# Kernel optimization log

Measured on AMD Instinct MI355X. Metric: run time of the kernel, lower is better.

## Reference

```python
import jax, jax.numpy as jnp
import numpy as np

B = 8192
TEXT_DIM = 2048
GRAPH_DIM = 1024
OUT_DIM = 1024
C = 2048  # common_dim = max(text_dim, graph_dim)
H = 16    # num_heads
LN_EPS = 1e-5


def _linear(x, W, b):
    # torch nn.Linear: y = x @ W.T + b, W: [out, in]
    return x @ W.T + b


def _mha(q, k, v, Wqkv, bqkv, Wo, bo):
    # Faithful to torch nn.MultiheadAttention (batch_first, eval mode).
    # Wqkv: [3C, C], bqkv: [3C], Wo: [C, C], bo: [C]
    Bq, S, _ = q.shape
    D = C // H
    Wq, Wk, Wv = Wqkv[:C], Wqkv[C:2 * C], Wqkv[2 * C:]
    bq, bk, bv = bqkv[:C], bqkv[C:2 * C], bqkv[2 * C:]
    qh = _linear(q, Wq, bq).reshape(Bq, S, H, D).transpose(0, 2, 1, 3)  # [B,H,S,D]
    kh = _linear(k, Wk, bk).reshape(Bq, S, H, D).transpose(0, 2, 1, 3)
    vh = _linear(v, Wv, bv).reshape(Bq, S, H, D).transpose(0, 2, 1, 3)
    scores = jnp.einsum('bhqd,bhkd->bhqk', qh, kh) / jnp.sqrt(jnp.asarray(D, qh.dtype))
    attn = jax.nn.softmax(scores, axis=-1)
    out = jnp.einsum('bhqk,bhkd->bhqd', attn, vh)
    out = out.transpose(0, 2, 1, 3).reshape(Bq, S, C)
    return _linear(out, Wo, bo)


def _layernorm(x, w, b):
    mu = jnp.mean(x, axis=-1, keepdims=True)
    var = jnp.mean(jnp.square(x - mu), axis=-1, keepdims=True)
    return (x - mu) * jax.lax.rsqrt(var + LN_EPS) * w + b


def setup_inputs() -> dict:
    key = jax.random.key(0)
    ks = jax.random.split(key, 16)
    s = 0.02
    return {
        'text_embeddings': jax.random.normal(ks[0], (B, TEXT_DIM), jnp.float32),
        'graph_embeddings': jax.random.normal(ks[1], (B, GRAPH_DIM), jnp.float32),
        'Wt': jax.random.normal(ks[2], (C, TEXT_DIM), jnp.float32) * s,
        'bt': jnp.zeros((C,), jnp.float32),
        'Wg': jax.random.normal(ks[3], (C, GRAPH_DIM), jnp.float32) * s,
        'bg': jnp.zeros((C,), jnp.float32),
        'Wqkv_s': jax.random.normal(ks[4], (3 * C, C), jnp.float32) * s,
        'bqkv_s': jnp.zeros((3 * C,), jnp.float32),
        'Wo_s': jax.random.normal(ks[5], (C, C), jnp.float32) * s,
        'bo_s': jnp.zeros((C,), jnp.float32),
        'Wqkv_c': jax.random.normal(ks[6], (3 * C, C), jnp.float32) * s,
        'bqkv_c': jnp.zeros((3 * C,), jnp.float32),
        'Wo_c': jax.random.normal(ks[7], (C, C), jnp.float32) * s,
        'bo_c': jnp.zeros((C,), jnp.float32),
        'ln_w': jnp.ones((C,), jnp.float32),
        'ln_b': jnp.zeros((C,), jnp.float32),
        'Wout': jax.random.normal(ks[8], (OUT_DIM, C), jnp.float32) * s,
        'bout': jnp.zeros((OUT_DIM,), jnp.float32),
    }


def reference(text_embeddings, graph_embeddings, Wt, bt, Wg, bg,
              Wqkv_s, bqkv_s, Wo_s, bo_s, Wqkv_c, bqkv_c, Wo_c, bo_c,
              ln_w, ln_b, Wout, bout):
    text_proj = _linear(text_embeddings, Wt, bt)    # [B, C]
    graph_proj = _linear(graph_embeddings, Wg, bg)  # [B, C]
    stacked = jnp.stack([text_proj, graph_proj], axis=1)  # [B, 2, C]
    attn_out = _mha(stacked, stacked, stacked, Wqkv_s, bqkv_s, Wo_s, bo_s)
    attn_out = _layernorm(attn_out, ln_w, ln_b)
    cross = _mha(attn_out, stacked, stacked, Wqkv_c, bqkv_c, Wo_c, bo_c)
    attn_out = attn_out + cross
    fused = jnp.mean(attn_out, axis=1)  # [B, C]
    return _linear(fused, Wout, bout)   # [B, OUT_DIM]
```

## Files before the change

kernel.cpp:

```cpp
#include <hip/hip_runtime.h>
#include <cstdio>

typedef unsigned short u16;
typedef float f32x4 __attribute__((ext_vector_type(4)));
typedef short s16x8 __attribute__((ext_vector_type(8)));

__device__ __forceinline__ u16 f2bf(float x) {
    unsigned u = __float_as_uint(x);
    u += 0x7fffu + ((u >> 16) & 1u);
    return (u16)(u >> 16);
}
__device__ __forceinline__ unsigned pack2(float a, float b) {
    return (unsigned)f2bf(a) | ((unsigned)f2bf(b) << 16);
}
__device__ __forceinline__ void unpack2(unsigned u, float& lo, float& hi) {
    lo = __uint_as_float(u << 16);
    hi = __uint_as_float(u & 0xffff0000u);
}

__device__ __forceinline__ void gl2lds16(const u16* g, u16* l) {
    __builtin_amdgcn_global_load_lds(
        (const __attribute__((address_space(1))) void*)g,
        (__attribute__((address_space(3))) void*)l, 16, 0, 0);
}

__device__ __forceinline__ uint4 ld8(const u16* p) { return *(const uint4*)p; }
__device__ __forceinline__ uint4 ld8(const float* p) {
    float4 a = ((const float4*)p)[0];
    float4 b = ((const float4*)p)[1];
    uint4 r;
    r.x = pack2(a.x, a.y);
    r.y = pack2(a.z, a.w);
    r.z = pack2(b.x, b.y);
    r.w = pack2(b.z, b.w);
    return r;
}

__global__ __launch_bounds__(256) void cast_f32_bf16(const float* __restrict__ x,
                                                     u16* __restrict__ y, int n4) {
    int i = blockIdx.x * 256 + threadIdx.x;
    if (i >= n4) return;
    float4 v = ((const float4*)x)[i];
    uint2 r;
    r.x = pack2(v.x, v.y);
    r.y = pack2(v.z, v.w);
    ((uint2*)y)[i] = r;
}

template <typename TA, typename TB, bool OUT_BF16>
__global__ __launch_bounds__(256) void gemm_bt(const TA* __restrict__ A,
                                               const TB* __restrict__ B,
                                               const float* __restrict__ bias,
                                               void* __restrict__ Cout,
                                               int K, int ldc) {
    __shared__ __align__(16) u16 As[128 * 32];
    __shared__ __align__(16) u16 Bs[128 * 32];

    const int tid = threadIdx.x;
    const int lane = tid & 63;
    const int wave = tid >> 6;
    const int wm = wave >> 1;
    const int wn = wave & 1;
    const size_t bm = (size_t)blockIdx.y * 128;
    const size_t bn = (size_t)blockIdx.x * 128;

    f32x4 acc[4][4];
#pragma unroll
    for (int i = 0; i < 4; ++i)
#pragma unroll
        for (int j = 0; j < 4; ++j) acc[i][j] = (f32x4)0.f;

    const int srow = tid >> 2;
    const int scol = (tid & 3) << 3;
    const TA* Ag = A + (bm + (size_t)srow) * K + scol;
    const TB* Bg = B + (bn + (size_t)srow) * K + scol;
    const size_t rstep = (size_t)64 * K;

    uint4 a0 = ld8(Ag);
    uint4 a1 = ld8(Ag + rstep);
    uint4 b0 = ld8(Bg);
    uint4 b1 = ld8(Bg + rstep);

    const int lrow = lane & 15;
    const int lk = (lane >> 4) << 3;

    const int niter = K >> 5;
    for (int t = 0; t < niter; ++t) {
        __syncthreads();
        *(uint4*)&As[srow * 32 + scol] = a0;
        *(uint4*)&As[(64 + srow) * 32 + scol] = a1;
        *(uint4*)&Bs[srow * 32 + scol] = b0;
        *(uint4*)&Bs[(64 + srow) * 32 + scol] = b1;
        __syncthreads();
        if (t + 1 < niter) {
            const int k0 = (t + 1) << 5;
            a0 = ld8(Ag + k0);
            a1 = ld8(Ag + rstep + k0);
            b0 = ld8(Bg + k0);
            b1 = ld8(Bg + rstep + k0);
        }
        s16x8 af[4], bfr[4];
#pragma unroll
        for (int i = 0; i < 4; ++i)
            af[i] = *(const s16x8*)&As[(wm * 64 + i * 16 + lrow) * 32 + lk];
#pragma unroll
        for (int j = 0; j < 4; ++j)
            bfr[j] = *(const s16x8*)&Bs[(wn * 64 + j * 16 + lrow) * 32 + lk];
#pragma unroll
        for (int i = 0; i < 4; ++i)
#pragma unroll
            for (int j = 0; j < 4; ++j)
                acc[i][j] = __builtin_amdgcn_mfma_f32_16x16x32_bf16(
                    af[i], bfr[j], acc[i][j], 0, 0, 0);
    }

    const size_t crow0 = bm + wm * 64 + ((lane >> 4) << 2);
    const int ccol0 = (int)bn + wn * 64 + (lane & 15);
#pragma unroll
    for (int i = 0; i < 4; ++i) {
#pragma unroll
        for (int j = 0; j < 4; ++j) {
            const int col = ccol0 + j * 16;
            const float bv = bias[col];
            const size_t base = (crow0 + (size_t)i * 16) * (size_t)ldc + col;
#pragma unroll
            for (int r = 0; r < 4; ++r) {
                const float v = acc[i][j][r] + bv;
                if (OUT_BF16)
                    ((u16*)Cout)[base + (size_t)r * ldc] = f2bf(v);
                else
                    ((float*)Cout)[base + (size_t)r * ldc] = v;
            }
        }
    }
}

template <bool OUT_BF16>
__global__ __launch_bounds__(256) void gemm_async(const u16* __restrict__ A, int lda,
                                                  const u16* __restrict__ B,
                                                  const float* __restrict__ bias,
                                                  void* __restrict__ Cout,
                                                  int K, int ldc) {
    __shared__ __align__(16) u16 As[128 * 32];
    __shared__ __align__(16) u16 Bs[128 * 32];

    const int tid = threadIdx.x;
    const int lane = tid & 63;
    const int wave = tid >> 6;
    const int wm = wave >> 1;
    const int wn = wave & 1;
    const size_t bm = (size_t)blockIdx.y * 128;
    const size_t bn = (size_t)blockIdx.x * 128;

    f32x4 acc[4][4];
#pragma unroll
    for (int i = 0; i < 4; ++i)
#pragma unroll
        for (int j = 0; j < 4; ++j) acc[i][j] = (f32x4)0.f;

    const int srow = tid >> 2;
    const int scol = (tid & 3) << 3;
    const u16* Ag = A + (bm + (size_t)srow) * (size_t)lda + scol;
    const u16* Bg = B + (bn + (size_t)srow) * (size_t)K + scol;
    const size_t rA = (size_t)64 * lda;
    const size_t rB = (size_t)64 * K;
    u16* lA0 = &As[tid * 8];
    u16* lA1 = &As[2048 + tid * 8];
    u16* lB0 = &Bs[tid * 8];
    u16* lB1 = &Bs[2048 + tid * 8];

    const int lrow = lane & 15;
    const int lk = (lane >> 4) << 3;

    const int niter = K >> 5;
    for (int t = 0; t < niter; ++t) {
        __syncthreads();
        gl2lds16(Ag, lA0);
        gl2lds16(Ag + rA, lA1);
        gl2lds16(Bg, lB0);
        gl2lds16(Bg + rB, lB1);
        Ag += 32;
        Bg += 32;
        __syncthreads();
        s16x8 af[4], bfr[4];
#pragma unroll
        for (int i = 0; i < 4; ++i)
            af[i] = *(const s16x8*)&As[(wm * 64 + i * 16 + lrow) * 32 + lk];
#pragma unroll
        for (int j = 0; j < 4; ++j)
            bfr[j] = *(const s16x8*)&Bs[(wn * 64 + j * 16 + lrow) * 32 + lk];
#pragma unroll
        for (int i = 0; i < 4; ++i)
#pragma unroll
            for (int j = 0; j < 4; ++j)
                acc[i][j] = __builtin_amdgcn_mfma_f32_16x16x32_bf16(
                    af[i], bfr[j], acc[i][j], 0, 0, 0);
    }

    const size_t crow0 = bm + wm * 64 + ((lane >> 4) << 2);
    const int ccol0 = (int)bn + wn * 64 + (lane & 15);
#pragma unroll
    for (int i = 0; i < 4; ++i) {
#pragma unroll
        for (int j = 0; j < 4; ++j) {
            const int col = ccol0 + j * 16;
            const float bv = bias[col];
            const size_t base = (crow0 + (size_t)i * 16) * (size_t)ldc + col;
#pragma unroll
            for (int r = 0; r < 4; ++r) {
                const float v = acc[i][j][r] + bv;
                if (OUT_BF16)
                    ((u16*)Cout)[base + (size_t)r * ldc] = f2bf(v);
                else
                    ((float*)Cout)[base + (size_t)r * ldc] = v;
            }
        }
    }
}

#define LDA_FRAG(mh)                                                          \
    do {                                                                      \
        _Pragma("unroll") for (int m = 0; m < 4; ++m) {                       \
            const u16* p = &As[cur][aBase + ((mh)*64 + m * 16) * 64];         \
            aF[m][0] = *(const s16x8*)(p + aK0);                              \
            aF[m][1] = *(const s16x8*)(p + aK1);                              \
        }                                                                     \
    } while (0)

#define LDB_FRAG(nh, bf)                                                      \
    do {                                                                      \
        _Pragma("unroll") for (int n = 0; n < 2; ++n) {                       \
            const u16* p = &Bs[cur][bBase + ((nh)*32 + n * 16) * 64];         \
            bf[n][0] = *(const s16x8*)(p + aK0);                              \
            bf[n][1] = *(const s16x8*)(p + aK1);                              \
        }                                                                     \
    } while (0)

#define STAGE_A(v, h)                                                         \
    do {                                                                      \
        u16* d = &As[(v)&1][(h)*8192 + tid * 8];                              \
        gl2lds16(aSrc[h][0] + (size_t)(v)*64, d);                             \
        gl2lds16(aSrc[h][1] + (size_t)(v)*64, d + 4096);                      \
    } while (0)

#define STAGE_B(v, h)                                                         \
    do {                                                                      \
        u16* d = &Bs[(v)&1][(h)*8192 + tid * 8];                              \
        gl2lds16(bSrc[h][0] + (size_t)(v)*64, d);                             \
        gl2lds16(bSrc[h][1] + (size_t)(v)*64, d + 4096);                      \
    } while (0)

#define MFMA_Q(mh, nh, bf)                                                    \
    do {                                                                      \
        __builtin_amdgcn_s_setprio(1);                                        \
        _Pragma("unroll") for (int m = 0; m < 4; ++m)                         \
            _Pragma("unroll") for (int n = 0; n < 2; ++n) {                   \
            acc[(mh)*4 + m][(nh)*2 + n] =                                     \
                __builtin_amdgcn_mfma_f32_16x16x32_bf16(                      \
                    aF[m][0], bf[n][0], acc[(mh)*4 + m][(nh)*2 + n], 0, 0, 0);\
            acc[(mh)*4 + m][(nh)*2 + n] =                                     \
                __builtin_amdgcn_mfma_f32_16x16x32_bf16(                      \
                    aF[m][1], bf[n][1], acc[(mh)*4 + m][(nh)*2 + n], 0, 0, 0);\
        }                                                                     \
        __builtin_amdgcn_s_setprio(0);                                        \
    } while (0)

#define TILE8(u, DO_A, DO_B, VM)                                              \
    do {                                                                      \
        const int cur = (u)&1;                                                \
                                                                      \
        LDA_FRAG(0);                                                          \
        LDB_FRAG(0, b0);                                                      \
        if (DO_A) STAGE_A((u) + 1, 0);                                        \
        __builtin_amdgcn_s_barrier();                                         \
        MFMA_Q(0, 0, b0);                                                     \
        __builtin_amdgcn_s_barrier();                                         \
                                                                      \
        LDB_FRAG(1, b1);                                                      \
        if (DO_A) STAGE_A((u) + 1, 1);                                        \
        __builtin_amdgcn_s_barrier();                                         \
        MFMA_Q(0, 1, b1);                                                     \
        __builtin_amdgcn_s_barrier();                                         \
                                                                      \
        LDA_FRAG(1);                                                          \
        if (DO_B) STAGE_B((u) + 2, 0);                                        \
        __builtin_amdgcn_s_barrier();                                         \
        MFMA_Q(1, 1, b1);                                                     \
        __builtin_amdgcn_s_barrier();                                         \
                                                                      \
        if (DO_B) STAGE_B((u) + 2, 1);                                        \
        if ((VM) == 4) asm volatile("s_waitcnt vmcnt(4)" ::: "memory");       \
        if ((VM) == 0) asm volatile("s_waitcnt vmcnt(0)" ::: "memory");       \
        __builtin_amdgcn_s_barrier();                                         \
        MFMA_Q(1, 0, b0);                                                     \
        __builtin_amdgcn_s_barrier();                                         \
    } while (0)

template <bool OUT_BF16>
__global__ __launch_bounds__(512, 2) void gemm8(const u16* __restrict__ A, int lda,
                                                const u16* __restrict__ B,
                                                const float* __restrict__ bias,
                                                void* __restrict__ Cout,
                                                int K, int ldc) {
    __shared__ __align__(16) u16 As[2][16384];
    __shared__ __align__(16) u16 Bs[2][16384];

    const int tid = threadIdx.x;
    const int lane = tid & 63;
    const int wave = tid >> 6;
    const int wm = wave >> 2;
    const int wn = wave & 3;

    const unsigned nwg = gridDim.x * gridDim.y;
    const unsigned orig = blockIdx.y * gridDim.x + blockIdx.x;
    const unsigned q = nwg >> 3, r = nwg & 7u;
    const unsigned xcd = orig & 7u, idx = orig >> 3;
    const unsigned wg =
        (xcd < r ? xcd * (q + 1) : r * (q + 1) + (xcd - r) * q) + idx;
    const size_t bm = (size_t)(wg / gridDim.x) * 256;
    const size_t bn = (size_t)(wg % gridDim.x) * 256;

    f32x4 acc[8][4];
#pragma unroll
    for (int i = 0; i < 8; ++i)
#pragma unroll
        for (int j = 0; j < 4; ++j) acc[i][j] = (f32x4)0.f;

    const int strow = tid >> 3;
    const int ssw = ((tid & 7) << 3) ^ ((strow & 7) << 3);
    const u16* aSrc[2][2];
    const u16* bSrc[2][2];
#pragma unroll
    for (int h = 0; h < 2; ++h)
#pragma unroll
        for (int e = 0; e < 2; ++e) {
            const int trow = h * 128 + e * 64 + strow;
            aSrc[h][e] = A + (bm + trow) * (size_t)lda + ssw;
            bSrc[h][e] = B + (bn + trow) * (size_t)K + ssw;
        }

    const int lrow = lane & 15;
    const int hi8 = (lane >> 4) << 3;
    const int fswz = (lrow & 7) << 3;
    const int aK0 = (0 + hi8) ^ fswz;
    const int aK1 = (32 + hi8) ^ fswz;
    const int aBase = (wm * 128 + lrow) * 64;
    const int bBase = (wn * 64 + lrow) * 64;

    s16x8 aF[4][2], b0[2][2], b1[2][2];

    const int NT = K >> 6;

    STAGE_A(0, 0);
    STAGE_A(0, 1);
    STAGE_B(0, 0);
    STAGE_B(0, 1);
    STAGE_B(1, 0);
    STAGE_B(1, 1);
    asm volatile("s_waitcnt vmcnt(4)" ::: "memory");
    __builtin_amdgcn_s_barrier();

    for (int u = 0; u < NT - 2; ++u) {
        TILE8(u, 1, 1, 4);
    }
    TILE8(NT - 2, 1, 0, 0);
    TILE8(NT - 1, 0, 0, -1);

    const size_t crow0 = bm + wm * 128 + ((lane >> 4) << 2);
    const int ccol0 = (int)bn + wn * 64 + (lane & 15);
#pragma unroll
    for (int im = 0; im < 8; ++im) {
#pragma unroll
        for (int in = 0; in < 4; ++in) {
            const int col = ccol0 + in * 16;
            const float bv = bias[col];
            const size_t base = (crow0 + (size_t)im * 16) * (size_t)ldc + col;
#pragma unroll
            for (int r = 0; r < 4; ++r) {
                const float v = acc[im][in][r] + bv;
                if (OUT_BF16)
                    ((u16*)Cout)[base + (size_t)r * ldc] = f2bf(v);
                else
                    ((float*)Cout)[base + (size_t)r * ldc] = v;
            }
        }
    }
}

#undef LDA_FRAG
#undef LDB_FRAG
#undef STAGE_A
#undef STAGE_B
#undef MFMA_Q
#undef TILE8

__device__ __forceinline__ void dot8(uint4 a, uint4 b, float& acc) {
    const unsigned* pa = (const unsigned*)&a;
    const unsigned* pb = (const unsigned*)&b;
#pragma unroll
    for (int i = 0; i < 4; ++i) {
        float alo, ahi, blo, bhi;
        unpack2(pa[i], alo, ahi);
        unpack2(pb[i], blo, bhi);
        acc += alo * blo + ahi * bhi;
    }
}

__global__ __launch_bounds__(256) void attn2(u16* __restrict__ qkv) {
    const int gid = blockIdx.x * 256 + threadIdx.x;
    const int b = gid >> 4;
    const int h = gid & 15;
    u16* base = qkv + (size_t)(2 * b) * 6144 + h * 128;
    float s00 = 0.f, s01 = 0.f, s10 = 0.f, s11 = 0.f;
#pragma unroll 4
    for (int c = 0; c < 128; c += 8) {
        uint4 q0 = *(const uint4*)(base + c);
        uint4 q1 = *(const uint4*)(base + 6144 + c);
        uint4 k0 = *(const uint4*)(base + 2048 + c);
        uint4 k1 = *(const uint4*)(base + 8192 + c);
        dot8(q0, k0, s00);
        dot8(q0, k1, s01);
        dot8(q1, k0, s10);
        dot8(q1, k1, s11);
    }
    const float scale = 0.0883883476483184f;
    s00 *= scale; s01 *= scale; s10 *= scale; s11 *= scale;
    const float m0 = fmaxf(s00, s01), m1 = fmaxf(s10, s11);
    const float e00 = __expf(s00 - m0), e01 = __expf(s01 - m0);
    const float e10 = __expf(s10 - m1), e11 = __expf(s11 - m1);
    const float r0 = 1.f / (e00 + e01), r1 = 1.f / (e10 + e11);
    const float p00 = e00 * r0, p01 = e01 * r0;
    const float p10 = e10 * r1, p11 = e11 * r1;

#pragma unroll 4
    for (int c = 0; c < 128; c += 8) {
        uint4 v0 = *(const uint4*)(base + 4096 + c);
        uint4 v1 = *(const uint4*)(base + 10240 + c);
        const unsigned* p0w = (const unsigned*)&v0;
        const unsigned* p1w = (const unsigned*)&v1;
        uint4 r0v, r1v;
        unsigned* q0w = (unsigned*)&r0v;
        unsigned* q1w = (unsigned*)&r1v;
#pragma unroll
        for (int i = 0; i < 4; ++i) {
            float v0lo, v0hi, v1lo, v1hi;
            unpack2(p0w[i], v0lo, v0hi);
            unpack2(p1w[i], v1lo, v1hi);
            q0w[i] = pack2(p00 * v0lo + p01 * v1lo, p00 * v0hi + p01 * v1hi);
            q1w[i] = pack2(p10 * v0lo + p11 * v1lo, p10 * v0hi + p11 * v1hi);
        }
        *(uint4*)(base + c) = r0v;
        *(uint4*)(base + 6144 + c) = r1v;
    }
}

__global__ __launch_bounds__(256) void ln_k(const u16* __restrict__ x, int ldx,
                                            const float* __restrict__ w,
                                            const float* __restrict__ bb,
                                            u16* __restrict__ y) {
    __shared__ float red[8];
    const int row = blockIdx.x;
    const int tid = threadIdx.x;
    const uint4 v = ((const uint4*)(x + (size_t)row * ldx))[tid];
    const unsigned* pw = (const unsigned*)&v;
    float f[8];
#pragma unroll
    for (int i = 0; i < 4; ++i) unpack2(pw[i], f[2 * i], f[2 * i + 1]);
    float s = 0.f, q = 0.f;
#pragma unroll
    for (int i = 0; i < 8; ++i) {
        s += f[i];
        q += f[i] * f[i];
    }
#pragma unroll
    for (int off = 32; off > 0; off >>= 1) {
        s += __shfl_down(s, off);
        q += __shfl_down(q, off);
    }
    if ((tid & 63) == 0) {
        red[tid >> 6] = s;
        red[4 + (tid >> 6)] = q;
    }
    __syncthreads();
    s = red[0] + red[1] + red[2] + red[3];
    q = red[4] + red[5] + red[6] + red[7];
    const float mu = s * (1.f / 2048.f);
    const float var = q * (1.f / 2048.f) - mu * mu;
    const float rstd = rsqrtf(var + 1e-5f);
    const float4 w0 = ((const float4*)w)[2 * tid];
    const float4 w1 = ((const float4*)w)[2 * tid + 1];
    const float4 b0 = ((const float4*)bb)[2 * tid];
    const float4 b1 = ((const float4*)bb)[2 * tid + 1];
    const float wv[8] = {w0.x, w0.y, w0.z, w0.w, w1.x, w1.y, w1.z, w1.w};
    const float bv[8] = {b0.x, b0.y, b0.z, b0.w, b1.x, b1.y, b1.z, b1.w};
    uint4 o;
    unsigned* po = (unsigned*)&o;
#pragma unroll
    for (int i = 0; i < 4; ++i) {
        float lo = (f[2 * i] - mu) * rstd * wv[2 * i] + bv[2 * i];
        float hi = (f[2 * i + 1] - mu) * rstd * wv[2 * i + 1] + bv[2 * i + 1];
        po[i] = pack2(lo, hi);
    }
    ((uint4*)(y + (size_t)row * 2048))[tid] = o;
}

__global__ __launch_bounds__(256) void mean_res(const u16* __restrict__ ln,
                                                const u16* __restrict__ co,
                                                u16* __restrict__ fused) {
    const int gid = blockIdx.x * 256 + threadIdx.x;
    const int b = gid >> 8;
    const int c8 = gid & 255;
    const uint4 l0 = ((const uint4*)(ln + (size_t)(2 * b) * 2048))[c8];
    const uint4 l1 = ((const uint4*)(ln + (size_t)(2 * b + 1) * 2048))[c8];
    const uint4 c0 = ((const uint4*)(co + (size_t)(2 * b) * 6144))[c8];
    const uint4 c1 = ((const uint4*)(co + (size_t)(2 * b + 1) * 6144))[c8];
    const unsigned* pl0 = (const unsigned*)&l0;
    const unsigned* pl1 = (const unsigned*)&l1;
    const unsigned* pc0 = (const unsigned*)&c0;
    const unsigned* pc1 = (const unsigned*)&c1;
    uint4 o;
    unsigned* po = (unsigned*)&o;
#pragma unroll
    for (int i = 0; i < 4; ++i) {
        float a_lo, a_hi, b_lo, b_hi, c_lo, c_hi, d_lo, d_hi;
        unpack2(pl0[i], a_lo, a_hi);
        unpack2(pl1[i], b_lo, b_hi);
        unpack2(pc0[i], c_lo, c_hi);
        unpack2(pc1[i], d_lo, d_hi);
        po[i] = pack2(0.5f * (a_lo + c_lo + b_lo + d_lo),
                      0.5f * (a_hi + c_hi + b_hi + d_hi));
    }
    ((uint4*)(fused + (size_t)b * 12288))[c8] = o;
}

extern "C" void kernel_launch(void* const* d_in, const int* in_sizes, int n_in,
                              void* d_out, int out_size, void* d_ws, size_t ws_size,
                              hipStream_t stream) {
    (void)in_sizes; (void)n_in; (void)out_size;
    const float* text   = (const float*)d_in[0];
    const float* graph  = (const float*)d_in[1];
    const float* Wt     = (const float*)d_in[2];
    const float* bt     = (const float*)d_in[3];
    const float* Wg     = (const float*)d_in[4];
    const float* bg     = (const float*)d_in[5];
    const float* Wqkv_s = (const float*)d_in[6];
    const float* bqkv_s = (const float*)d_in[7];
    const float* Wo_s   = (const float*)d_in[8];
    const float* bo_s   = (const float*)d_in[9];
    const float* Wqkv_c = (const float*)d_in[10];
    const float* bqkv_c = (const float*)d_in[11];
    const float* Wo_c   = (const float*)d_in[12];
    const float* bo_c   = (const float*)d_in[13];
    const float* ln_w   = (const float*)d_in[14];
    const float* ln_b   = (const float*)d_in[15];
    const float* Wout   = (const float*)d_in[16];
    const float* bout   = (const float*)d_in[17];
    float* out = (float*)d_out;

    char* ws = (char*)d_ws;
    u16* wQs  = (u16*)ws;
    u16* wQc  = wQs + 12582912ull;
    u16* wOs  = wQc + 12582912ull;
    u16* wOc  = wOs + 4194304ull;
    u16* wWt  = wOc + 4194304ull;
    u16* wWg  = wWt + 4194304ull;
    u16* wOut = wWg + 2097152ull;
    const size_t WB = 83886080ull;

    size_t CH = 8192;
    while (CH > 128 && WB + 40960ull * CH > ws_size) CH >>= 1;
    fprintf(stderr, "[kernel_launch] ws_size=%zu need=%zu CH=%zu\n",
            ws_size, WB + 40960ull * CH, CH);
    if (WB + 40960ull * CH > ws_size || d_ws == nullptr) return;

    const size_t T = 2 * CH;
    char* ca = ws + WB;
    u16* stacked_c = (u16*)ca;
    u16* ln_c      = (u16*)(ca + 4096 * T);
    u16* qkv_c     = (u16*)(ca + 8192 * T);

    auto cast = [&](const float* x, u16* y, size_t n) {
        int n4 = (int)(n >> 2);
        cast_f32_bf16<<<(n4 + 255) / 256, 256, 0, stream>>>(x, y, n4);
    };
    cast(Wqkv_s, wQs, 12582912ull);
    cast(Wqkv_c, wQc, 12582912ull);
    cast(Wo_s, wOs, 4194304ull);
    cast(Wo_c, wOc, 4194304ull);
    cast(Wt, wWt, 4194304ull);
    cast(Wg, wWg, 2097152ull);
    cast(Wout, wOut, 2097152ull);

    const dim3 blk(256);
    const dim3 blk8(512);
    const unsigned gy  = (unsigned)(CH / 128);
    const unsigned g8  = (unsigned)(T / 256);

    for (size_t c0 = 0; c0 < 8192; c0 += CH) {
        gemm_bt<float, u16, true><<<dim3(16, gy), blk, 0, stream>>>(
            text + c0 * 2048, wWt, bt, stacked_c, 2048, 4096);
        gemm_bt<float, u16, true><<<dim3(16, gy), blk, 0, stream>>>(
            graph + c0 * 1024, wWg, bg, stacked_c + 2048, 1024, 4096);
        gemm8<true><<<dim3(24, g8), blk8, 0, stream>>>(
            stacked_c, 2048, wQs, bqkv_s, qkv_c, 2048, 6144);
        attn2<<<(unsigned)(CH / 16), blk, 0, stream>>>(qkv_c);
        gemm8<true><<<dim3(8, g8), blk8, 0, stream>>>(
            qkv_c, 6144, wOs, bo_s, qkv_c + 4096, 2048, 6144);
        ln_k<<<(unsigned)T, blk, 0, stream>>>(qkv_c + 4096, 6144, ln_w, ln_b, ln_c);
        gemm8<true><<<dim3(8, g8), blk8, 0, stream>>>(
            ln_c, 2048, wQc, bqkv_c, qkv_c, 2048, 6144);
        gemm8<true><<<dim3(16, g8), blk8, 0, stream>>>(
            stacked_c, 2048, wQc + 2048ull * 2048, bqkv_c + 2048,
            qkv_c + 2048, 2048, 6144);
        attn2<<<(unsigned)(CH / 16), blk, 0, stream>>>(qkv_c);
        gemm8<true><<<dim3(8, g8), blk8, 0, stream>>>(
            qkv_c, 6144, wOc, bo_c, qkv_c + 4096, 2048, 6144);
        mean_res<<<(unsigned)CH, blk, 0, stream>>>(ln_c, qkv_c + 4096, qkv_c);
        gemm_async<false><<<dim3(8, gy), blk, 0, stream>>>(
            qkv_c, 12288, wOut, bout, out + c0 * 1024, 2048, 1024);
    }
}
```

Baseline: 2.072 ms.

## Restructure gemm8 main loop to interleave LDS fragment reads with MFMAs

Rewrites the 256x256 bf16 GEMM inner loop. LDS fragment reads for the next A half and the next tile's A/B fragments are now interleaved with the MFMA groups, and the global-to-LDS staging is split into finer quarter chunks spread across the phases. This is meant to hide LDS read latency behind matrix work and cut the number of barriers per K-tile from eight to four. The cost is more complex vmcnt bookkeeping, where a wrong count could race, and possibly higher register pressure from holding prefetched fragments.

```diff
diff --git a/kernel.cpp b/kernel.cpp
--- a/kernel.cpp
+++ b/kernel.cpp
@@ -218,81 +218,96 @@
     }
 }
 
-#define LDA_FRAG(mh)                                                          \
-    do {                                                                      \
+#define STG_A02(v)                                                            \
+    do {                                                                      \
+        gl2lds16(aG + (size_t)(v) * 64, &As[(v) & 1][tid * 8]);               \
+        gl2lds16(aG + 2 * a64 + (size_t)(v) * 64,                             \
+                 &As[(v) & 1][8192 + tid * 8]);                               \
+    } while (0)
+#define STG_A13(v)                                                            \
+    do {                                                                      \
+        gl2lds16(aG + a64 + (size_t)(v) * 64, &As[(v) & 1][4096 + tid * 8]);  \
+        gl2lds16(aG + 3 * a64 + (size_t)(v) * 64,                             \
+                 &As[(v) & 1][12288 + tid * 8]);                              \
+    } while (0)
+#define STG_B01(v)                                                            \
+    do {                                                                      \
+        gl2lds16(bG + (size_t)(v) * 64, &Bs[(v) & 1][tid * 8]);               \
+        gl2lds16(bG + b64 + (size_t)(v) * 64, &Bs[(v) & 1][4096 + tid * 8]);  \
+    } while (0)
+#define STG_B23(v)                                                            \
+    do {                                                                      \
+        gl2lds16(bG + 2 * b64 + (size_t)(v) * 64,                             \
+                 &Bs[(v) & 1][8192 + tid * 8]);                               \
+        gl2lds16(bG + 3 * b64 + (size_t)(v) * 64,                             \
+                 &Bs[(v) & 1][12288 + tid * 8]);                              \
+    } while (0)
+#define RD_AF(buf, mh, m)                                                     \
+    do {                                                                      \
+        const u16* p_ = &As[buf][aRow + ((mh) * 64 + (m) * 16) * 64];         \
+        aF[m][0] = *(const s16x8*)(p_ + aK0);                                 \
+        aF[m][1] = *(const s16x8*)(p_ + aK1);                                 \
+    } while (0)
+#define RD_B(buf, nh, dst)                                                    \
+    do {                                                                      \
+        _Pragma("unroll") for (int n_ = 0; n_ < 2; ++n_) {                    \
+            const u16* p_ = &Bs[buf][bRow + ((nh) * 32 + n_ * 16) * 64];      \
+            dst[n_][0] = *(const s16x8*)(p_ + aK0);                           \
+            dst[n_][1] = *(const s16x8*)(p_ + aK1);                           \
+        }                                                                     \
+    } while (0)
+#define MFMA4(ar, bv, ci, cj)                                                 \
+    do {                                                                      \
+        acc[ci][cj] = __builtin_amdgcn_mfma_f32_16x16x32_bf16(                \
+            (ar)[0], (bv)[0], acc[ci][cj], 0, 0, 0);                          \
+        acc[ci][cj] = __builtin_amdgcn_mfma_f32_16x16x32_bf16(                \
+            (ar)[1], (bv)[1], acc[ci][cj], 0, 0, 0);                          \
+    } while (0)
+
+#define TILEW(u, SA13, S2, RDN, V2S, V4S)                                     \
+    do {                                                                      \
+        const int cur = (u) & 1, oth = cur ^ 1;                               \
+                                                          \
+        if (SA13) STG_A13((u) + 1);                                           \
+        RD_B(cur, 1, b1);                                                     \
+        __builtin_amdgcn_s_setprio(1);                                        \
         _Pragma("unroll") for (int m = 0; m < 4; ++m) {                       \
-            const u16* p = &As[cur][aBase + ((mh)*64 + m * 16) * 64];         \
-            aF[m][0] = *(const s16x8*)(p + aK0);                              \
-            aF[m][1] = *(const s16x8*)(p + aK1);                              \
-        }                                                                     \
-    } while (0)
-
-#define LDB_FRAG(nh, bf)                                                      \
-    do {                                                                      \
-        _Pragma("unroll") for (int n = 0; n < 2; ++n) {                       \
-            const u16* p = &Bs[cur][bBase + ((nh)*32 + n * 16) * 64];         \
-            bf[n][0] = *(const s16x8*)(p + aK0);                              \
-            bf[n][1] = *(const s16x8*)(p + aK1);                              \
-        }                                                                     \
-    } while (0)
-
-#define STAGE_A(v, h)                                                         \
-    do {                                                                      \
-        u16* d = &As[(v)&1][(h)*8192 + tid * 8];                              \
-        gl2lds16(aSrc[h][0] + (size_t)(v)*64, d);                             \
-        gl2lds16(aSrc[h][1] + (size_t)(v)*64, d + 4096);                      \
-    } while (0)
-
-#define STAGE_B(v, h)                                                         \
-    do {                                                                      \
-        u16* d = &Bs[(v)&1][(h)*8192 + tid * 8];                              \
-        gl2lds16(bSrc[h][0] + (size_t)(v)*64, d);                             \
-        gl2lds16(bSrc[h][1] + (size_t)(v)*64, d + 4096);                      \
-    } while (0)
-
-#define MFMA_Q(mh, nh, bf)                                                    \
-    do {                                                                      \
-        __builtin_amdgcn_s_setprio(1);                                        \
-        _Pragma("unroll") for (int m = 0; m < 4; ++m)                         \
-            _Pragma("unroll") for (int n = 0; n < 2; ++n) {                   \
-            acc[(mh)*4 + m][(nh)*2 + n] =                                     \
-                __builtin_amdgcn_mfma_f32_16x16x32_bf16(                      \
-                    aF[m][0], bf[n][0], acc[(mh)*4 + m][(nh)*2 + n], 0, 0, 0);\
-            acc[(mh)*4 + m][(nh)*2 + n] =                                     \
-                __builtin_amdgcn_mfma_f32_16x16x32_bf16(                      \
-                    aF[m][1], bf[n][1], acc[(mh)*4 + m][(nh)*2 + n], 0, 0, 0);\
+            MFMA4(aF[m], b0[0], m, 0);                                        \
+            MFMA4(aF[m], b0[1], m, 1);                                        \
         }                                                                     \
         __builtin_amdgcn_s_setprio(0);                                        \
-    } while (0)
-
-#define TILE8(u, DO_A, DO_B, VM)                                              \
-    do {                                                                      \
-        const int cur = (u)&1;                                                \
-                                                                      \
-        LDA_FRAG(0);                                                          \
-        LDB_FRAG(0, b0);                                                      \
-        if (DO_A) STAGE_A((u) + 1, 0);                                        \
+        asm volatile("s_waitcnt " V2S ::: "memory");                          \
         __builtin_amdgcn_s_barrier();                                         \
-        MFMA_Q(0, 0, b0);                                                     \
+                                  \
+        if (S2) STG_A02((u) + 2);                                             \
+        __builtin_amdgcn_s_setprio(1);                                        \
+        _Pragma("unroll") for (int m = 0; m < 4; ++m) {                       \
+            MFMA4(aF[m], b1[0], m, 2);                                        \
+            MFMA4(aF[m], b1[1], m, 3);                                        \
+            RD_AF(cur, 1, m);                                                 \
+        }                                                                     \
+        __builtin_amdgcn_s_setprio(0);                                        \
         __builtin_amdgcn_s_barrier();                                         \
-                                                                      \
-        LDB_FRAG(1, b1);                                                      \
-        if (DO_A) STAGE_A((u) + 1, 1);                                        \
+                                                          \
+        if (S2) STG_B01((u) + 2);                                             \
+        __builtin_amdgcn_s_setprio(1);                                        \
+        _Pragma("unroll") for (int m = 0; m < 4; ++m) {                       \
+            MFMA4(aF[m], b1[0], 4 + m, 2);                                    \
+            MFMA4(aF[m], b1[1], 4 + m, 3);                                    \
+        }                                                                     \
+        __builtin_amdgcn_s_setprio(0);                                        \
+        asm volatile("s_waitcnt " V4S ::: "memory");                          \
         __builtin_amdgcn_s_barrier();                                         \
-        MFMA_Q(0, 1, b1);                                                     \
-        __builtin_amdgcn_s_barrier();                                         \
-                                                                      \
-        LDA_FRAG(1);                                                          \
-        if (DO_B) STAGE_B((u) + 2, 0);                                        \
-        __builtin_amdgcn_s_barrier();                                         \
-        MFMA_Q(1, 1, b1);                                                     \
-        __builtin_amdgcn_s_barrier();                                         \
-                                                                      \
-        if (DO_B) STAGE_B((u) + 2, 1);                                        \
-        if ((VM) == 4) asm volatile("s_waitcnt vmcnt(4)" ::: "memory");       \
-        if ((VM) == 0) asm volatile("s_waitcnt vmcnt(0)" ::: "memory");       \
-        __builtin_amdgcn_s_barrier();                                         \
-        MFMA_Q(1, 0, b0);                                                     \
+                         \
+        if (S2) STG_B23((u) + 2);                                             \
+        __builtin_amdgcn_s_setprio(1);                                        \
+        _Pragma("unroll") for (int m = 0; m < 4; ++m) {                       \
+            MFMA4(aF[m], b0[0], 4 + m, 0);                                    \
+            MFMA4(aF[m], b0[1], 4 + m, 1);                                    \
+            if (RDN) RD_AF(oth, 0, m);                                        \
+        }                                                                     \
+        __builtin_amdgcn_s_setprio(0);                                        \
+        if (RDN) RD_B(oth, 0, b0);                                            \
         __builtin_amdgcn_s_barrier();                                         \
     } while (0)
 
@@ -328,43 +343,40 @@
 
     const int strow = tid >> 3;
     const int ssw = ((tid & 7) << 3) ^ ((strow & 7) << 3);
-    const u16* aSrc[2][2];
-    const u16* bSrc[2][2];
-#pragma unroll
-    for (int h = 0; h < 2; ++h)
-#pragma unroll
-        for (int e = 0; e < 2; ++e) {
-            const int trow = h * 128 + e * 64 + strow;
-            aSrc[h][e] = A + (bm + trow) * (size_t)lda + ssw;
-            bSrc[h][e] = B + (bn + trow) * (size_t)K + ssw;
-        }
+    const u16* aG = A + (bm + (size_t)strow) * (size_t)lda + ssw;
+    const u16* bG = B + (bn + (size_t)strow) * (size_t)K + ssw;
+    const size_t a64 = (size_t)64 * lda;
+    const size_t b64 = (size_t)64 * K;
 
     const int lrow = lane & 15;
     const int hi8 = (lane >> 4) << 3;
     const int fswz = (lrow & 7) << 3;
-    const int aK0 = (0 + hi8) ^ fswz;
+    const int aK0 = hi8 ^ fswz;
     const int aK1 = (32 + hi8) ^ fswz;
-    const int aBase = (wm * 128 + lrow) * 64;
-    const int bBase = (wn * 64 + lrow) * 64;
+    const int aRow = (wm * 128 + lrow) * 64;
+    const int bRow = (wn * 64 + lrow) * 64;
 
     s16x8 aF[4][2], b0[2][2], b1[2][2];
 
     const int NT = K >> 6;
 
-    STAGE_A(0, 0);
-    STAGE_A(0, 1);
-    STAGE_B(0, 0);
-    STAGE_B(0, 1);
-    STAGE_B(1, 0);
-    STAGE_B(1, 1);
-    asm volatile("s_waitcnt vmcnt(4)" ::: "memory");
+    STG_A02(0);
+    STG_A13(0);
+    STG_B01(0);
+    STG_B23(0);
+    STG_A02(1);
+    STG_B01(1);
+    STG_B23(1);
+    asm volatile("s_waitcnt vmcnt(6)" ::: "memory");
     __builtin_amdgcn_s_barrier();
-
-    for (int u = 0; u < NT - 2; ++u) {
-        TILE8(u, 1, 1, 4);
-    }
-    TILE8(NT - 2, 1, 0, 0);
-    TILE8(NT - 1, 0, 0, -1);
+#pragma unroll
+    for (int m = 0; m < 4; ++m) RD_AF(0, 0, m);
+    RD_B(0, 0, b0);
+
+    for (int u = 0; u < NT - 2; ++u)
+        TILEW(u, 1, 1, 1, "vmcnt(8)", "vmcnt(6)");
+    TILEW(NT - 2, 1, 0, 1, "vmcnt(8)", "vmcnt(2)");
+    TILEW(NT - 1, 0, 0, 0, "vmcnt(0)", "vmcnt(0)");
 
     const size_t crow0 = bm + wm * 128 + ((lane >> 4) << 2);
     const int ccol0 = (int)bn + wn * 64 + (lane & 15);
@@ -387,12 +399,14 @@
     }
 }
 
-#undef LDA_FRAG
-#undef LDB_FRAG
-#undef STAGE_A
-#undef STAGE_B
-#undef MFMA_Q
-#undef TILE8
+#undef STG_A02
+#undef STG_A13
+#undef STG_B01
+#undef STG_B23
+#undef RD_AF
+#undef RD_B
+#undef MFMA4
+#undef TILEW
 
 __device__ __forceinline__ void dot8(uint4 a, uint4 b, float& acc) {
     const unsigned* pa = (const unsigned*)&a;
```

New measurement: 1.955 ms. 1.06x faster.
